# Kernel tuning notes

Hardware: AMD Instinct MI355X
Metric: run time of the kernel (lower is better)

## Reference

```python
import jax, jax.numpy as jnp
import numpy as np

N_NODES = 100000
N_EDGES = 1600000
IN_C = 64
HID = 64
OUT_C = 40


def setup_inputs() -> dict:
    key = jax.random.key(0)
    ks = jax.random.split(key, 12)
    def lin_init(k, fan_in, shape):
        bound = 1.0 / np.sqrt(fan_in)
        return jax.random.uniform(k, shape, jnp.float32, -bound, bound)
    x0 = jax.random.normal(ks[0], (N_NODES, IN_C), jnp.float32)
    edge_index = jax.random.randint(ks[1], (2, N_EDGES), 0, N_NODES, jnp.int64)
    return {
        "x0": x0,
        "edge_index": edge_index,
        "W1": lin_init(ks[2], IN_C, (HID, IN_C)),
        "b1": lin_init(ks[3], IN_C, (HID,)),
        "Wr1": lin_init(ks[4], IN_C, (HID, IN_C)),
        "br1": lin_init(ks[5], IN_C, (HID,)),
        "W2": lin_init(ks[6], HID, (HID, HID)),
        "b2": lin_init(ks[7], HID, (HID,)),
        "Wr2": lin_init(ks[8], HID, (HID, HID)),
        "br2": lin_init(ks[9], HID, (HID,)),
        "Wl": lin_init(ks[10], 2 * HID, (OUT_C, 2 * HID)),
        "bl": lin_init(ks[11], 2 * HID, (OUT_C,)),
    }


def _norm_weights(row, col, num_nodes):
    # symmetric degree normalization: d^-1/2[row] * d^-1/2[col]
    ones = jnp.ones(row.shape[0], jnp.float32)
    deg = jax.ops.segment_sum(ones, row, num_segments=num_nodes)
    dis = jnp.where(deg > 0, jax.lax.rsqrt(jnp.maximum(deg, 1.0)) * jnp.where(deg > 0, 1.0, 0.0), 0.0)
    dis = jnp.where(deg > 0, deg ** -0.5, 0.0)
    return dis[row] * dis[col]


def _bigraph_conv(x, row, col, w, W, b, Wr, br, num_nodes):
    h = x @ W.T + b                                    # [N, out]
    msg = w[:, None] * h[col]                          # gather + scale, [E, out]
    agg = jax.ops.segment_sum(msg, row, num_segments=num_nodes)
    return agg + x @ Wr.T + br


def reference(x0, edge_index, W1, b1, Wr1, br1, W2, b2, Wr2, br2, Wl, bl):
    num_nodes = x0.shape[0]
    row, col = edge_index[0], edge_index[1]
    w = _norm_weights(row, col, num_nodes)
    x1 = jax.nn.relu(_bigraph_conv(x0, row, col, w, W1, b1, Wr1, br1, num_nodes))
    x2 = jax.nn.relu(_bigraph_conv(x1, row, col, w, W2, b2, Wr2, br2, num_nodes))
    x = jnp.concatenate([x1, x2], axis=-1)
    logits = x @ Wl.T + bl
    return jax.nn.log_softmax(logits, axis=-1)
```

## Files before the change

kernel.cpp:

```cpp
#include <hip/hip_runtime.h>
#include <math.h>


typedef unsigned short u16;
typedef unsigned int   u32;

#define BROWS 512
#define BIN_CHUNK 8192
#define CAPB 12288

__device__ __forceinline__ u16 f2bf(float f) {
  u32 u = __float_as_uint(f);
  u32 r = u + 0x7fffu + ((u >> 16) & 1u);
  return (u16)(r >> 16);
}
__device__ __forceinline__ float bf2f(u16 h) {
  return __uint_as_float(((u32)h) << 16);
}

__global__ __launch_bounds__(256) void k_binA(
    const int* __restrict__ row, const int* __restrict__ col,
    unsigned* __restrict__ bCnt, unsigned* __restrict__ pairs,
    int nE, int NB, int capA)
{
  __shared__ unsigned cnt[256], base[256], gb[256], sc[256];
  __shared__ unsigned buf[BIN_CHUNK];
  const int t = threadIdx.x;
  const int tb = blockIdx.x * BIN_CHUNK;

  cnt[t] = 0;
  __syncthreads();

  unsigned pk[32];
  unsigned short po[32];
  short bk[32];
#pragma unroll
  for (int j = 0; j < 32; ++j) {
    int i = tb + j * 256 + t;
    if (i < nE) {
      int r = row[i], c = col[i];
      int b = r >> 9;
      pk[j] = ((unsigned)(r & (BROWS - 1)) << 17) | (unsigned)c;
      bk[j] = (short)b;
      po[j] = (unsigned short)atomicAdd(&cnt[b], 1u);
    } else bk[j] = -1;
  }
  __syncthreads();
  sc[t] = cnt[t];
  __syncthreads();
  for (int off = 1; off < 256; off <<= 1) {
    unsigned v = (t >= off) ? sc[t - off] : 0u;
    __syncthreads();
    sc[t] += v;
    __syncthreads();
  }
  base[t] = t ? sc[t - 1] : 0u;
  __syncthreads();
#pragma unroll
  for (int j = 0; j < 32; ++j)
    if (bk[j] >= 0) buf[base[bk[j]] + po[j]] = pk[j];
  unsigned c = cnt[t];
  gb[t] = c ? atomicAdd(&bCnt[t], c) : 0u;
  __syncthreads();
  for (int b = 0; b < NB; ++b) {
    unsigned cb = cnt[b];
    if (!cb) continue;
    unsigned lo = base[b], g = gb[b];
    size_t dst = (size_t)b * (unsigned)capA;
    for (unsigned u = t; u < cb; u += 256)
      if (g + u < (unsigned)capA) pairs[dst + g + u] = buf[lo + u];
  }
}

__global__ __launch_bounds__(256) void k_bscan(const unsigned* __restrict__ bCnt,
                                               unsigned* __restrict__ bBase, int NB) {
  __shared__ unsigned sc[256];
  int t = threadIdx.x;
  unsigned v = (t < NB) ? min(bCnt[t], (unsigned)CAPB) : 0u;
  sc[t] = v;
  __syncthreads();
  for (int off = 1; off < 256; off <<= 1) {
    unsigned u = (t >= off) ? sc[t - off] : 0u;
    __syncthreads();
    sc[t] += u;
    __syncthreads();
  }
  if (t < NB) bBase[t] = t ? sc[t - 1] : 0u;
}

__global__ __launch_bounds__(256) void k_binB(
    const unsigned* __restrict__ pairs, const unsigned* __restrict__ bCnt,
    const unsigned* __restrict__ bBase, int* __restrict__ colS,
    unsigned* __restrict__ start, float* __restrict__ dis,
    int N, int capA)
{
  __shared__ unsigned hist[BROWS], ex[BROWS], cur[BROWS], sc[256];
  __shared__ unsigned cols[CAPB];
  const int t = threadIdx.x;
  const int b = blockIdx.x;
  const unsigned cnt = min(bCnt[b], (unsigned)CAPB);
  const unsigned gbase = bBase[b];
  const size_t src = (size_t)b * (unsigned)capA;

  hist[t] = 0; hist[256 + t] = 0;
  __syncthreads();
  for (unsigned i = t; i < cnt; i += 256)
    atomicAdd(&hist[pairs[src + i] >> 17], 1u);
  __syncthreads();
  unsigned h0 = hist[2 * t], h1 = hist[2 * t + 1];
  sc[t] = h0 + h1;
  __syncthreads();
  for (int off = 1; off < 256; off <<= 1) {
    unsigned v = (t >= off) ? sc[t - off] : 0u;
    __syncthreads();
    sc[t] += v;
    __syncthreads();
  }
  unsigned bexc = t ? sc[t - 1] : 0u;
  ex[2 * t] = bexc;          cur[2 * t] = bexc;
  ex[2 * t + 1] = bexc + h0; cur[2 * t + 1] = bexc + h0;
  __syncthreads();
  for (unsigned i = t; i < cnt; i += 256) {
    unsigned p = pairs[src + i];
    unsigned pos = atomicAdd(&cur[p >> 17], 1u);
    cols[pos] = p & 0x1FFFFu;
  }
  __syncthreads();
  for (unsigned i = t; i < cnt; i += 256)
    colS[gbase + i] = (int)cols[i];
  const int rowBase = b * BROWS;
#pragma unroll
  for (int j = 0; j < BROWS / 256; ++j) {
    int lr = j * 256 + t;
    int n = rowBase + lr;
    if (n < N) {
      unsigned d = hist[lr];
      start[n] = gbase + ex[lr] + d;
      dis[n] = d ? rsqrtf((float)d) : 0.f;
    }
  }
}

__global__ __launch_bounds__(256) void k_deg(const int* __restrict__ row,
                                             unsigned* __restrict__ deg, int nE) {
  int i = blockIdx.x * blockDim.x + threadIdx.x;
  int stride = gridDim.x * blockDim.x;
  for (; i < nE; i += stride) atomicAdd(&deg[row[i]], 1u);
}

__global__ __launch_bounds__(256) void k_dis(const unsigned* __restrict__ deg,
                                             float* __restrict__ dis, int n) {
  int i = blockIdx.x * blockDim.x + threadIdx.x;
  if (i < n) {
    unsigned d = deg[i];
    dis[i] = d > 0u ? rsqrtf((float)d) : 0.f;
  }
}

__global__ __launch_bounds__(256) void k_scan1(const unsigned* __restrict__ deg,
                                               unsigned* __restrict__ start,
                                               unsigned* __restrict__ bsum, int n) {
  __shared__ unsigned s[256];
  const int base = blockIdx.x * 2048;
  unsigned v[8], tsum = 0;
#pragma unroll
  for (int j = 0; j < 8; ++j) {
    int idx = base + threadIdx.x * 8 + j;
    v[j] = idx < n ? deg[idx] : 0u;
    tsum += v[j];
  }
  s[threadIdx.x] = tsum;
  __syncthreads();
  for (int off = 1; off < 256; off <<= 1) {
    unsigned t = (threadIdx.x >= off) ? s[threadIdx.x - off] : 0u;
    __syncthreads();
    s[threadIdx.x] += t;
    __syncthreads();
  }
  unsigned run = threadIdx.x ? s[threadIdx.x - 1] : 0u;
  if (threadIdx.x == 255) bsum[blockIdx.x] = s[255];
#pragma unroll
  for (int j = 0; j < 8; ++j) {
    int idx = base + threadIdx.x * 8 + j;
    if (idx < n) start[idx] = run;
    run += v[j];
  }
}

__global__ void k_scan2(unsigned* __restrict__ bsum, int nB) {
  if (threadIdx.x == 0 && blockIdx.x == 0) {
    unsigned run = 0;
    for (int b = 0; b < nB; ++b) { unsigned t = bsum[b]; bsum[b] = run; run += t; }
  }
}

__global__ __launch_bounds__(256) void k_scan3(unsigned* __restrict__ start,
                                               const unsigned* __restrict__ bsum, int n) {
  int i = blockIdx.x * blockDim.x + threadIdx.x;
  if (i < n) start[i] += bsum[i >> 11];
}

__global__ __launch_bounds__(256) void k_build(const int* __restrict__ row,
                                               const int* __restrict__ col,
                                               unsigned* __restrict__ start,
                                               int* __restrict__ colS, int nE) {
  int i = blockIdx.x * blockDim.x + threadIdx.x;
  int stride = gridDim.x * blockDim.x;
  for (; i < nE; i += stride) {
    int r = row[i];
    unsigned p = atomicAdd(&start[r], 1u);
    colS[p] = col[i];
  }
}

__global__ __launch_bounds__(256) void k_cast(const float4* __restrict__ x4,
                                              ushort4* __restrict__ out, int n4) {
  int i = blockIdx.x * blockDim.x + threadIdx.x;
  int stride = gridDim.x * blockDim.x;
  for (; i < n4; i += stride) {
    float4 f = x4[i];
    ushort4 v;
    v.x = f2bf(f.x); v.y = f2bf(f.y); v.z = f2bf(f.z); v.w = f2bf(f.w);
    out[i] = v;
  }
}

__global__ __launch_bounds__(256) void k_prep(
    const float* __restrict__ W1, const float* __restrict__ b1,
    const float* __restrict__ Wr1, const float* __restrict__ br1,
    const float* __restrict__ W2, const float* __restrict__ b2,
    const float* __restrict__ Wr2, const float* __restrict__ br2,
    float4* __restrict__ UT)
{
  int i = blockIdx.x * 256 + threadIdx.x;
  if (i >= 2 * 33 * 64) return;
  int layer = i / (33 * 64);
  int kq = (i / 64) % 33;
  int o = i % 64;
  const float* W  = layer ? W2  : W1;
  const float* Wr = layer ? Wr2 : Wr1;
  const float* b  = layer ? b2  : b1;
  const float* br = layer ? br2 : br1;
  float4 v;
  if (kq < 16)       v = ((const float4*)W)[o * 16 + kq];
  else if (kq < 32)  v = ((const float4*)Wr)[o * 16 + kq - 16];
  else               v = make_float4(b[o], br[o], 0.f, 0.f);
  UT[i] = v;
}

__global__ __launch_bounds__(256) void k_spmm_h(
    const u16* __restrict__ xh, u16* __restrict__ aggh, float* __restrict__ rs,
    const int* __restrict__ colS, const unsigned* __restrict__ startEnd,
    const float* __restrict__ dis, int nNodes)
{
  const int t = threadIdx.x, wave = t >> 6, lane = t & 63;
  const int g = lane >> 4, sub = lane & 15;
  const int n = blockIdx.x * 4 + wave;
  if (n >= nNodes) return;
  const unsigned lo = n ? startEnd[n - 1] : 0u;
  const unsigned hi = startEnd[n];
  const ushort4* h4 = (const ushort4*)xh;
  float ax = 0.f, ay = 0.f, az = 0.f, aw = 0.f, sw = 0.f;
  for (unsigned base = lo; base < hi; base += 64) {
    const int cnt = (int)min(64u, hi - base);
    int   myc = (lane < cnt) ? colS[base + lane] : 0;
    float myw = (lane < cnt) ? dis[myc] : 0.f;
    sw += myw;
    for (int j = 0; j < cnt; j += 16) {
      int ja = j + g, jb = j + 4 + g, jc = j + 8 + g, jd = j + 12 + g;
      int   c0 = __shfl(myc, ja); float w0 = __shfl(myw, ja);
      int   c1 = __shfl(myc, jb); float w1 = __shfl(myw, jb);
      int   c2 = __shfl(myc, jc); float w2 = __shfl(myw, jc);
      int   c3 = __shfl(myc, jd); float w3 = __shfl(myw, jd);
      ushort4 v0 = h4[(size_t)c0 * 16 + sub];
      ushort4 v1 = h4[(size_t)c1 * 16 + sub];
      ushort4 v2 = h4[(size_t)c2 * 16 + sub];
      ushort4 v3 = h4[(size_t)c3 * 16 + sub];
      ax += w0 * bf2f(v0.x) + w1 * bf2f(v1.x) + w2 * bf2f(v2.x) + w3 * bf2f(v3.x);
      ay += w0 * bf2f(v0.y) + w1 * bf2f(v1.y) + w2 * bf2f(v2.y) + w3 * bf2f(v3.y);
      az += w0 * bf2f(v0.z) + w1 * bf2f(v1.z) + w2 * bf2f(v2.z) + w3 * bf2f(v3.z);
      aw += w0 * bf2f(v0.w) + w1 * bf2f(v1.w) + w2 * bf2f(v2.w) + w3 * bf2f(v3.w);
    }
  }
  ax += __shfl_xor(ax, 16); ay += __shfl_xor(ay, 16);
  az += __shfl_xor(az, 16); aw += __shfl_xor(aw, 16);
  ax += __shfl_xor(ax, 32); ay += __shfl_xor(ay, 32);
  az += __shfl_xor(az, 32); aw += __shfl_xor(aw, 32);
  sw += __shfl_xor(sw, 1);  sw += __shfl_xor(sw, 2);
  sw += __shfl_xor(sw, 4);  sw += __shfl_xor(sw, 8);
  sw += __shfl_xor(sw, 16); sw += __shfl_xor(sw, 32);
  const float dn = dis[n];
  if (lane < 16) {
    ushort4 o;
    o.x = f2bf(dn * ax); o.y = f2bf(dn * ay);
    o.z = f2bf(dn * az); o.w = f2bf(dn * aw);
    ((ushort4*)aggh)[(size_t)n * 16 + sub] = o;
  }
  if (lane == 0) rs[n] = dn * sw;
}

__global__ __launch_bounds__(256) void k_gemv(
    const u16* __restrict__ aggh, const float* __restrict__ rs,
    const u16* __restrict__ rooth, const float4* __restrict__ UT,
    u16* __restrict__ xo, int nNodes)
{
  __shared__ u16 xsh[64][136];
  const int t = threadIdx.x;
  const int lane = t & 63;
  const int og = __builtin_amdgcn_readfirstlane(t >> 6);
  const int n0 = blockIdx.x * 64;

  {
    const int r = t >> 2, q = t & 3;
    int gn = n0 + r; if (gn > nNodes - 1) gn = nNodes - 1;
    const uint4* a = (const uint4*)(aggh + (size_t)gn * 64);
    const uint4* x = (const uint4*)(rooth + (size_t)gn * 64);
    *(uint4*)&xsh[r][q * 16]           = a[q * 2];
    *(uint4*)&xsh[r][q * 16 + 8]       = a[q * 2 + 1];
    *(uint4*)&xsh[r][64 + q * 16]      = x[q * 2];
    *(uint4*)&xsh[r][64 + q * 16 + 8]  = x[q * 2 + 1];
  }
  __syncthreads();

  float acc[16];
#pragma unroll
  for (int j = 0; j < 16; ++j) acc[j] = 0.f;

#pragma unroll 4
  for (int k = 0; k < 32; ++k) {
    ushort4 v = *(const ushort4*)&xsh[lane][k * 4];
    float xa = bf2f(v.x), xb = bf2f(v.y), xc = bf2f(v.z), xd = bf2f(v.w);
    const float4* w = UT + k * 64 + og * 16;
#pragma unroll
    for (int j = 0; j < 16; ++j) {
      float4 W = w[j];
      acc[j] = fmaf(xa, W.x, fmaf(xb, W.y, fmaf(xc, W.z, fmaf(xd, W.w, acc[j]))));
    }
  }

  const int n = n0 + lane;
  const float rsv = (n < nNodes) ? rs[n] : 0.f;
  {
    const float4* w = UT + 32 * 64 + og * 16;
#pragma unroll
    for (int j = 0; j < 16; ++j) {
      float4 W = w[j];
      acc[j] = fmaf(rsv, W.x, acc[j]) + W.y;
    }
  }

  if (n < nNodes) {
    uint4 u0, u1;
    u0.x = (u32)f2bf(fmaxf(acc[0], 0.f))  | ((u32)f2bf(fmaxf(acc[1], 0.f)) << 16);
    u0.y = (u32)f2bf(fmaxf(acc[2], 0.f))  | ((u32)f2bf(fmaxf(acc[3], 0.f)) << 16);
    u0.z = (u32)f2bf(fmaxf(acc[4], 0.f))  | ((u32)f2bf(fmaxf(acc[5], 0.f)) << 16);
    u0.w = (u32)f2bf(fmaxf(acc[6], 0.f))  | ((u32)f2bf(fmaxf(acc[7], 0.f)) << 16);
    u1.x = (u32)f2bf(fmaxf(acc[8], 0.f))  | ((u32)f2bf(fmaxf(acc[9], 0.f)) << 16);
    u1.y = (u32)f2bf(fmaxf(acc[10], 0.f)) | ((u32)f2bf(fmaxf(acc[11], 0.f)) << 16);
    u1.z = (u32)f2bf(fmaxf(acc[12], 0.f)) | ((u32)f2bf(fmaxf(acc[13], 0.f)) << 16);
    u1.w = (u32)f2bf(fmaxf(acc[14], 0.f)) | ((u32)f2bf(fmaxf(acc[15], 0.f)) << 16);
    uint4* dst = (uint4*)(xo + (size_t)n * 64 + og * 16);
    dst[0] = u0;
    dst[1] = u1;
  }
}

__global__ __launch_bounds__(256) void k_final(
    const u16* __restrict__ x1h, const u16* __restrict__ x2h,
    const float* __restrict__ Wl, const float* __restrict__ bl,
    float* __restrict__ out, int nNodes)
{
  __shared__ float4 xs[64][33];
  __shared__ float redM[64][4];
  __shared__ float redS[64][4];
  const int t = threadIdx.x;
  const int lane = t & 63;
  const int og = __builtin_amdgcn_readfirstlane(t >> 6);
  const int nodeBase = blockIdx.x * 64;

  {
    const int sn = t >> 2, q = t & 3;
    int gn = nodeBase + sn;
    if (gn > nNodes - 1) gn = nNodes - 1;
    const ushort4* a = (q < 2) ? (const ushort4*)(x1h + (size_t)gn * 64)
                               : (const ushort4*)(x2h + (size_t)gn * 64);
    const int qq = q & 1;
#pragma unroll
    for (int j = 0; j < 8; ++j) {
      ushort4 v = a[qq * 8 + j];
      xs[sn][q * 8 + j] = make_float4(bf2f(v.x), bf2f(v.y), bf2f(v.z), bf2f(v.w));
    }
  }
  __syncthreads();

  const float4* W4 = (const float4*)Wl;
  float acc[10];
#pragma unroll
  for (int j = 0; j < 10; ++j) acc[j] = bl[og * 10 + j];
  for (int k = 0; k < 32; ++k) {
    float4 x = xs[lane][k];
#pragma unroll
    for (int j = 0; j < 10; ++j) {
      float4 w = W4[(og * 10 + j) * 32 + k];
      acc[j] += w.x * x.x + w.y * x.y + w.z * x.z + w.w * x.w;
    }
  }

  float m10 = acc[0];
#pragma unroll
  for (int j = 1; j < 10; ++j) m10 = fmaxf(m10, acc[j]);
  redM[lane][og] = m10;
  __syncthreads();
  float M = fmaxf(fmaxf(redM[lane][0], redM[lane][1]),
                  fmaxf(redM[lane][2], redM[lane][3]));
  float s10 = 0.f;
#pragma unroll
  for (int j = 0; j < 10; ++j) s10 += __expf(acc[j] - M);
  redS[lane][og] = s10;
  __syncthreads();
  const float S = redS[lane][0] + redS[lane][1] + redS[lane][2] + redS[lane][3];
  const float lse = M + __logf(S);

  const int n = nodeBase + lane;
  if (n < nNodes) {
    float2* o2 = (float2*)(out + (size_t)n * 40 + og * 10);
#pragma unroll
    for (int q = 0; q < 5; ++q)
      o2[q] = make_float2(acc[2 * q] - lse, acc[2 * q + 1] - lse);
  }
}

extern "C" void kernel_launch(void* const* d_in, const int* in_sizes, int n_in,
                              void* d_out, int out_size, void* d_ws, size_t ws_size,
                              hipStream_t stream) {
  const float* x0  = (const float*)d_in[0];
  const int*   ei  = (const int*)d_in[1];
  const float* W1  = (const float*)d_in[2];
  const float* b1  = (const float*)d_in[3];
  const float* Wr1 = (const float*)d_in[4];
  const float* br1 = (const float*)d_in[5];
  const float* W2  = (const float*)d_in[6];
  const float* b2  = (const float*)d_in[7];
  const float* Wr2 = (const float*)d_in[8];
  const float* br2 = (const float*)d_in[9];
  const float* Wl  = (const float*)d_in[10];
  const float* bl  = (const float*)d_in[11];
  float* out = (float*)d_out;

  const int N = in_sizes[0] / 64;
  const int E = in_sizes[1] / 2;
  const int* row = ei;
  const int* col = ei + E;

  const int NB = (N + BROWS - 1) / BROWS;
  const int capA = 16384;
  const int avg = E / (NB > 0 ? NB : 1);
  const bool binOK = (N <= 131072) && (NB <= 256) &&
                     (avg + 12 * (int)sqrtf((float)avg + 1.f) + 256 <= CAPB);

  size_t P = (size_t)NB * capA;
  if (P < (size_t)32 * N) P = (size_t)32 * N;

  const size_t UT_W = 2 * 33 * 64 * 4;
  const size_t needBin = 4 * (512 + P + (size_t)E + (size_t)3 * N + UT_W +
                              (size_t)32 * N + (size_t)32 * N);
  const size_t needCSR = 4 * ((size_t)4 * N + 64 + (size_t)E + UT_W +
                              (size_t)32 * N + (size_t)32 * N + (size_t)32 * N);

  unsigned *start = nullptr; float *dis = nullptr, *rsv = nullptr;
  int* colS = nullptr; float4* UT = nullptr;
  u16 *aggh = nullptr, *x0h = nullptr, *x1h = nullptr, *x2h = nullptr;
  bool ok = false;

  if (binOK && ws_size >= needBin) {
    unsigned* bCnt  = (unsigned*)d_ws;
    unsigned* bBase = bCnt + 256;
    unsigned* pairs = bBase + 256;
    colS  = (int*)(pairs + P);
    start = (unsigned*)(colS + E);
    dis   = (float*)(start + N);
    rsv   = dis + N;
    UT    = (float4*)(rsv + N);
    aggh  = (u16*)(UT + 2 * 33 * 64);
    x1h   = aggh + (size_t)64 * N;
    x0h   = (u16*)pairs;
    x2h   = (u16*)pairs;

    hipMemsetAsync(bCnt, 0, 256 * 4, stream);
    k_binA<<<(E + BIN_CHUNK - 1) / BIN_CHUNK, 256, 0, stream>>>(row, col, bCnt, pairs, E, NB, capA);
    k_bscan<<<1, 256, 0, stream>>>(bCnt, bBase, NB);
    k_binB<<<NB, 256, 0, stream>>>(pairs, bCnt, bBase, colS, start, dis, N, capA);
    ok = true;
  } else if (ws_size >= needCSR) {
    unsigned* deg = (unsigned*)d_ws;
    start = deg + N;
    dis   = (float*)(start + N);
    rsv   = dis + N;
    unsigned* bsum = (unsigned*)(rsv + N);
    colS  = (int*)(bsum + 64);
    UT    = (float4*)(colS + E);
    aggh  = (u16*)(UT + 2 * 33 * 64);
    x1h   = aggh + (size_t)64 * N;
    u16* xsh = x1h + (size_t)64 * N;
    x0h = xsh; x2h = xsh;

    const int nB = (N + 2047) / 2048;
    hipMemsetAsync(deg, 0, (size_t)N * 4, stream);
    k_deg<<<1024, 256, 0, stream>>>(row, deg, E);
    k_dis<<<(N + 255) / 256, 256, 0, stream>>>(deg, dis, N);
    k_scan1<<<nB, 256, 0, stream>>>(deg, start, bsum, N);
    k_scan2<<<1, 64, 0, stream>>>(bsum, nB);
    k_scan3<<<(N + 255) / 256, 256, 0, stream>>>(start, bsum, N);
    k_build<<<1024, 256, 0, stream>>>(row, col, start, colS, E);
    ok = true;
  }

  if (!ok) return;

  k_cast<<<1024, 256, 0, stream>>>((const float4*)x0, (ushort4*)x0h, N * 16);
  k_prep<<<17, 256, 0, stream>>>(W1, b1, Wr1, br1, W2, b2, Wr2, br2, UT);

  k_spmm_h<<<(N + 3) / 4, 256, 0, stream>>>(x0h, aggh, rsv, colS, start, dis, N);
  k_gemv<<<(N + 63) / 64, 256, 0, stream>>>(aggh, rsv, x0h, UT, x1h, N);

  k_spmm_h<<<(N + 3) / 4, 256, 0, stream>>>(x1h, aggh, rsv, colS, start, dis, N);
  k_gemv<<<(N + 63) / 64, 256, 0, stream>>>(aggh, rsv, x1h, UT + 33 * 64, x2h, N);

  k_final<<<(N + 63) / 64, 256, 0, stream>>>(x1h, x2h, Wl, bl, out, N);
}
```

Before: 270.8 us.

## Widen binning kernels with per-wave shared counters and 1024/512-thread blocks

The first binning kernel now runs 1024 threads per block. Each thread handles 8 edges instead of 32, and the block keeps per-wave histograms so shared-memory atomic contention drops. The histograms are merged with a per-bucket prefix over waves, and the bucket flush to global memory is spread one wave per bucket. The second binning kernel uses 512 threads so each thread owns one row of the 512-row histogram and scan. The cost is a longer scan and more barriers with mostly idle threads in the reduction, plus extra shared memory for the 16x256 counters.

```diff
diff --git a/kernel.cpp b/kernel.cpp
--- a/kernel.cpp
+++ b/kernel.cpp
@@ -18,56 +18,74 @@
   return __uint_as_float(((u32)h) << 16);
 }
 
-__global__ __launch_bounds__(256) void k_binA(
+__global__ __launch_bounds__(1024) void k_binA(
     const int* __restrict__ row, const int* __restrict__ col,
     unsigned* __restrict__ bCnt, unsigned* __restrict__ pairs,
     int nE, int NB, int capA)
 {
-  __shared__ unsigned cnt[256], base[256], gb[256], sc[256];
   __shared__ unsigned buf[BIN_CHUNK];
+  __shared__ unsigned cnt[16][256];
+  __shared__ unsigned base[256], gb[256], tot[256], sc[256];
   const int t = threadIdx.x;
+  const int wave = t >> 6, lane = t & 63;
   const int tb = blockIdx.x * BIN_CHUNK;
 
-  cnt[t] = 0;
-  __syncthreads();
-
-  unsigned pk[32];
-  unsigned short po[32];
-  short bk[32];
-#pragma unroll
-  for (int j = 0; j < 32; ++j) {
-    int i = tb + j * 256 + t;
+  for (int i = t; i < 16 * 256; i += 1024) ((unsigned*)cnt)[i] = 0;
+  __syncthreads();
+
+  unsigned pk[8];
+  unsigned short po[8];
+  short bk[8];
+#pragma unroll
+  for (int j = 0; j < 8; ++j) {
+    int i = tb + j * 1024 + t;
     if (i < nE) {
       int r = row[i], c = col[i];
       int b = r >> 9;
       pk[j] = ((unsigned)(r & (BROWS - 1)) << 17) | (unsigned)c;
       bk[j] = (short)b;
-      po[j] = (unsigned short)atomicAdd(&cnt[b], 1u);
+      po[j] = (unsigned short)atomicAdd(&cnt[wave][b], 1u);
     } else bk[j] = -1;
   }
   __syncthreads();
-  sc[t] = cnt[t];
+
+  if (t < 256) {
+    unsigned run = 0;
+#pragma unroll
+    for (int w = 0; w < 16; ++w) {
+      unsigned c = cnt[w][t];
+      cnt[w][t] = run;
+      run += c;
+    }
+    tot[t] = run;
+    sc[t] = run;
+  }
   __syncthreads();
   for (int off = 1; off < 256; off <<= 1) {
-    unsigned v = (t >= off) ? sc[t - off] : 0u;
-    __syncthreads();
-    sc[t] += v;
-    __syncthreads();
-  }
-  base[t] = t ? sc[t - 1] : 0u;
-  __syncthreads();
-#pragma unroll
-  for (int j = 0; j < 32; ++j)
-    if (bk[j] >= 0) buf[base[bk[j]] + po[j]] = pk[j];
-  unsigned c = cnt[t];
-  gb[t] = c ? atomicAdd(&bCnt[t], c) : 0u;
-  __syncthreads();
-  for (int b = 0; b < NB; ++b) {
-    unsigned cb = cnt[b];
+    unsigned v = 0;
+    if (t < 256 && t >= off) v = sc[t - off];
+    __syncthreads();
+    if (t < 256) sc[t] += v;
+    __syncthreads();
+  }
+  if (t < 256) {
+    base[t] = t ? sc[t - 1] : 0u;
+    unsigned c = tot[t];
+    gb[t] = c ? atomicAdd(&bCnt[t], c) : 0u;
+  }
+  __syncthreads();
+
+#pragma unroll
+  for (int j = 0; j < 8; ++j)
+    if (bk[j] >= 0) buf[base[bk[j]] + cnt[wave][bk[j]] + po[j]] = pk[j];
+  __syncthreads();
+
+  for (int b = wave; b < NB; b += 16) {
+    unsigned cb = tot[b];
     if (!cb) continue;
     unsigned lo = base[b], g = gb[b];
     size_t dst = (size_t)b * (unsigned)capA;
-    for (unsigned u = t; u < cb; u += 256)
+    for (unsigned u = lane; u < cb; u += 64)
       if (g + u < (unsigned)capA) pairs[dst + g + u] = buf[lo + u];
   }
 }
@@ -88,13 +106,13 @@
   if (t < NB) bBase[t] = t ? sc[t - 1] : 0u;
 }
 
-__global__ __launch_bounds__(256) void k_binB(
+__global__ __launch_bounds__(512) void k_binB(
     const unsigned* __restrict__ pairs, const unsigned* __restrict__ bCnt,
     const unsigned* __restrict__ bBase, int* __restrict__ colS,
     unsigned* __restrict__ start, float* __restrict__ dis,
     int N, int capA)
 {
-  __shared__ unsigned hist[BROWS], ex[BROWS], cur[BROWS], sc[256];
+  __shared__ unsigned hist[BROWS], ex[BROWS], cur[BROWS], sc[BROWS];
   __shared__ unsigned cols[CAPB];
   const int t = threadIdx.x;
   const int b = blockIdx.x;
@@ -102,42 +120,35 @@
   const unsigned gbase = bBase[b];
   const size_t src = (size_t)b * (unsigned)capA;
 
-  hist[t] = 0; hist[256 + t] = 0;
-  __syncthreads();
-  for (unsigned i = t; i < cnt; i += 256)
+  hist[t] = 0;
+  __syncthreads();
+  for (unsigned i = t; i < cnt; i += 512)
     atomicAdd(&hist[pairs[src + i] >> 17], 1u);
   __syncthreads();
-  unsigned h0 = hist[2 * t], h1 = hist[2 * t + 1];
-  sc[t] = h0 + h1;
-  __syncthreads();
-  for (int off = 1; off < 256; off <<= 1) {
+  const unsigned h = hist[t];
+  sc[t] = h;
+  __syncthreads();
+  for (int off = 1; off < 512; off <<= 1) {
     unsigned v = (t >= off) ? sc[t - off] : 0u;
     __syncthreads();
     sc[t] += v;
     __syncthreads();
   }
-  unsigned bexc = t ? sc[t - 1] : 0u;
-  ex[2 * t] = bexc;          cur[2 * t] = bexc;
-  ex[2 * t + 1] = bexc + h0; cur[2 * t + 1] = bexc + h0;
-  __syncthreads();
-  for (unsigned i = t; i < cnt; i += 256) {
+  const unsigned e = sc[t] - h;
+  ex[t] = e; cur[t] = e;
+  __syncthreads();
+  for (unsigned i = t; i < cnt; i += 512) {
     unsigned p = pairs[src + i];
     unsigned pos = atomicAdd(&cur[p >> 17], 1u);
     cols[pos] = p & 0x1FFFFu;
   }
   __syncthreads();
-  for (unsigned i = t; i < cnt; i += 256)
+  for (unsigned i = t; i < cnt; i += 512)
     colS[gbase + i] = (int)cols[i];
-  const int rowBase = b * BROWS;
-#pragma unroll
-  for (int j = 0; j < BROWS / 256; ++j) {
-    int lr = j * 256 + t;
-    int n = rowBase + lr;
-    if (n < N) {
-      unsigned d = hist[lr];
-      start[n] = gbase + ex[lr] + d;
-      dis[n] = d ? rsqrtf((float)d) : 0.f;
-    }
+  const int n = b * BROWS + t;
+  if (n < N) {
+    start[n] = gbase + e + h;
+    dis[n] = h ? rsqrtf((float)h) : 0.f;
   }
 }
 
@@ -487,9 +498,9 @@
     x2h   = (u16*)pairs;
 
     hipMemsetAsync(bCnt, 0, 256 * 4, stream);
-    k_binA<<<(E + BIN_CHUNK - 1) / BIN_CHUNK, 256, 0, stream>>>(row, col, bCnt, pairs, E, NB, capA);
+    k_binA<<<(E + BIN_CHUNK - 1) / BIN_CHUNK, 1024, 0, stream>>>(row, col, bCnt, pairs, E, NB, capA);
     k_bscan<<<1, 256, 0, stream>>>(bCnt, bBase, NB);
-    k_binB<<<NB, 256, 0, stream>>>(pairs, bCnt, bBase, colS, start, dis, N, capA);
+    k_binB<<<NB, 512, 0, stream>>>(pairs, bCnt, bBase, colS, start, dis, N, capA);
     ok = true;
   } else if (ws_size >= needCSR) {
     unsigned* deg = (unsigned*)d_ws;
```

New measurement: 225.0 us. 1.2x faster.
